# Performance work log

Measured on AMD Instinct MI355X. Metric: run time of the kernel, lower is better.

## Reference

```python
import jax, jax.numpy as jnp
import numpy as np

N_NODES = 100000
N_EDGES = 1600000
F_IN = 256
F_OUT = 128


def setup_inputs() -> dict:
    key = jax.random.key(0)
    k1, k2, k3, k4, k5 = jax.random.split(key, 5)
    x = jax.random.normal(k1, (N_NODES, F_IN), dtype=jnp.float32)
    edge_src = jax.random.randint(k2, (N_EDGES,), 0, N_NODES, dtype=jnp.int64)
    edge_dst = jax.random.randint(k3, (N_EDGES,), 0, N_NODES, dtype=jnp.int64)
    edge_vals = jax.random.uniform(k4, (N_EDGES,), dtype=jnp.float32)
    kernel = jax.random.normal(k5, (F_IN, F_OUT), dtype=jnp.float32) * (1.0 / np.sqrt(F_IN))
    bias = jnp.zeros((F_OUT,), dtype=jnp.float32)
    return {"x": x, "edge_src": edge_src, "edge_dst": edge_dst,
            "edge_vals": edge_vals, "kernel": kernel, "bias": bias}


def reference(x, edge_src, edge_dst, edge_vals, kernel, bias):
    # h = x @ kernel  (dense feature transform), [N, F_OUT]
    h = x @ kernel
    # output = adj @ h  (sparse aggregation over COO edges)
    # message for edge e: adj[dst, src] * h[src]
    msg = h[edge_src] * edge_vals[:, None]          # [E, F_OUT]
    out = jax.ops.segment_sum(msg, edge_dst, num_segments=N_NODES)
    return out + bias
```

## Files before the change

### kernel.cpp

```cpp
#include <hip/hip_runtime.h>

constexpr int F_IN  = 256;
constexpr int F_OUT = 128;

constexpr int BSHIFT = 6;
constexpr int SUPSH  = 5;
constexpr int NPSH   = BSHIFT + SUPSH;
constexpr int NPS    = 1 << NPSH;
constexpr int EPT    = 16;
constexpr int BATCH  = 256 * EPT;
constexpr int CAPS   = 40960;

typedef __attribute__((ext_vector_type(8))) short short8;
typedef __attribute__((ext_vector_type(4))) float f32x4;

__device__ __forceinline__ unsigned short f2bf(float f) {
    unsigned u = __float_as_uint(f);
    u += 0x7fffu + ((u >> 16) & 1u);
    return (unsigned short)(u >> 16);
}

__global__ void prep_wt_kernel(const float* __restrict__ W,
                               unsigned short* __restrict__ Wt,
                               int* __restrict__ cursorA)
{
    int n = blockIdx.x;
    int k = threadIdx.x;
    int ks = k >> 5, kk = k & 31;
    Wt[((ks * F_OUT) + n) * 32 + kk] = f2bf(W[k * F_OUT + n]);
    if (blockIdx.x == 0 && threadIdx.x < 64) cursorA[threadIdx.x] = threadIdx.x * CAPS;
}

#define BS_LD 40

__global__ __launch_bounds__(256) void gemm_mfma_kernel(
    const float* __restrict__ x, const unsigned short* __restrict__ Wt,
    unsigned short* __restrict__ h, int n_nodes)
{
    __shared__ unsigned short Bs[F_OUT * BS_LD];

    const int tid  = threadIdx.x;
    const int wave = tid >> 6;
    const int lane = tid & 63;
    const int m16  = lane & 15;
    const int quad = lane >> 4;
    const int k0q  = quad * 8;
    const int arow = blockIdx.x * 64 + wave * 16 + m16;
    const bool inb = arow < n_nodes;

    f32x4 acc[8];
    #pragma unroll
    for (int t = 0; t < 8; ++t) acc[t] = (f32x4)(0.f);

    float4 a0 = make_float4(0.f,0.f,0.f,0.f), a1 = a0;
    if (inb) {
        a0 = *(const float4*)&x[(long long)arow * F_IN + k0q];
        a1 = *(const float4*)&x[(long long)arow * F_IN + k0q + 4];
    }

    for (int ks = 0; ks < 8; ++ks) {
        const uint4* wsrc = (const uint4*)(Wt + (size_t)ks * F_OUT * 32);
        #pragma unroll
        for (int p = 0; p < 2; ++p) {
            int c   = p * 256 + tid;
            int row = c >> 2;
            int o16 = c & 3;
            *(uint4*)&Bs[row * BS_LD + o16 * 8] = wsrc[c];
        }
        __syncthreads();

        short8 af;
        af[0] = (short)f2bf(a0.x); af[1] = (short)f2bf(a0.y);
        af[2] = (short)f2bf(a0.z); af[3] = (short)f2bf(a0.w);
        af[4] = (short)f2bf(a1.x); af[5] = (short)f2bf(a1.y);
        af[6] = (short)f2bf(a1.z); af[7] = (short)f2bf(a1.w);
        if (!inb) af = (short8)0;

        if (ks < 7 && inb) {
            int kn = (ks + 1) * 32 + k0q;
            a0 = *(const float4*)&x[(long long)arow * F_IN + kn];
            a1 = *(const float4*)&x[(long long)arow * F_IN + kn + 4];
        }

        #pragma unroll
        for (int t = 0; t < 8; ++t) {
            int n = t * 16 + m16;
            short8 bf = *(const short8*)&Bs[n * BS_LD + k0q];
            acc[t] = __builtin_amdgcn_mfma_f32_16x16x32_bf16(af, bf, acc[t], 0, 0, 0);
        }
        __syncthreads();
    }

    const int rbase = blockIdx.x * 64 + wave * 16 + quad * 4;
    #pragma unroll
    for (int r = 0; r < 4; ++r) {
        int grow = rbase + r;
        if (grow < n_nodes) {
            #pragma unroll
            for (int t = 0; t < 8; ++t)
                h[(long long)grow * F_OUT + t * 16 + m16] = f2bf(acc[t][r]);
        }
    }
}

__global__ __launch_bounds__(256) void partition_a_kernel(
    const int* __restrict__ src, const int* __restrict__ dst,
    const float* __restrict__ vals, int* __restrict__ cursorA,
    uint2* __restrict__ payA, int n_edges)
{
    __shared__ int hist[64];
    __shared__ int base[64];
    const int tid = threadIdx.x;
    const int i0  = blockIdx.x * BATCH;

    if (tid < 64) hist[tid] = 0;
    __syncthreads();

    uint2 p[EPT];
    int   sb[EPT];
    int   rk[EPT];
    #pragma unroll
    for (int j = 0; j < EPT; ++j) {
        int i = i0 + j * 256 + tid;
        sb[j] = -1;
        if (i < n_edges) {
            int d = dst[i];
            p[j] = make_uint2((unsigned)src[i] | ((unsigned)(d & (NPS - 1)) << 17),
                              __float_as_uint(vals[i]));
            sb[j] = d >> NPSH;
            rk[j] = atomicAdd(&hist[sb[j]], 1);
        }
    }
    __syncthreads();
    if (tid < 64) { int v = hist[tid]; if (v) base[tid] = atomicAdd(&cursorA[tid], v); }
    __syncthreads();
    #pragma unroll
    for (int j = 0; j < EPT; ++j)
        if (sb[j] >= 0) payA[base[sb[j]] + rk[j]] = p[j];
}

__global__ __launch_bounds__(512) void sort_super_kernel(
    const uint2* __restrict__ payA, const int* __restrict__ super_end,
    uint2* __restrict__ sorted, int* __restrict__ offsets, int n_nodes)
{
    __shared__ int bins[NPS];
    __shared__ int bcur[NPS];
    __shared__ int ss[512];

    const int sp  = blockIdx.x;
    const int tid = threadIdx.x;
    const int lo  = sp * CAPS;
    const int hi  = super_end[sp];

    for (int i = tid; i < NPS; i += 512) bins[i] = 0;
    __syncthreads();

    {
        int e = lo + tid;
        for (; e + 3 * 512 < hi; e += 4 * 512) {
            unsigned x0 = payA[e].x, x1 = payA[e + 512].x,
                     x2 = payA[e + 1024].x, x3 = payA[e + 1536].x;
            atomicAdd(&bins[(x0 >> 17) & (NPS - 1)], 1);
            atomicAdd(&bins[(x1 >> 17) & (NPS - 1)], 1);
            atomicAdd(&bins[(x2 >> 17) & (NPS - 1)], 1);
            atomicAdd(&bins[(x3 >> 17) & (NPS - 1)], 1);
        }
        for (; e < hi; e += 512)
            atomicAdd(&bins[(payA[e].x >> 17) & (NPS - 1)], 1);
    }
    __syncthreads();

    const int b4 = tid * 4;
    int c0 = bins[b4], c1 = bins[b4 + 1], c2 = bins[b4 + 2], c3 = bins[b4 + 3];
    int tot = c0 + c1 + c2 + c3;
    ss[tid] = tot;
    __syncthreads();
    for (int off = 1; off < 512; off <<= 1) {
        int v = (tid >= off) ? ss[tid - off] : 0;
        __syncthreads();
        ss[tid] += v;
        __syncthreads();
    }
    int run = lo + ss[tid] - tot;
    bcur[b4]     = run;
    bcur[b4 + 1] = run + c0;
    bcur[b4 + 2] = run + c0 + c1;
    bcur[b4 + 3] = run + c0 + c1 + c2;
    __syncthreads();

    const int node0 = sp << NPSH;
    for (int i = tid; i < NPS; i += 512) {
        int nd = node0 + i;
        if (nd < n_nodes) offsets[nd] = bcur[i];
    }
    __syncthreads();

    {
        int e = lo + tid;
        for (; e + 3 * 512 < hi; e += 4 * 512) {
            uint2 p0 = payA[e], p1 = payA[e + 512], p2 = payA[e + 1024], p3 = payA[e + 1536];
            int q0 = atomicAdd(&bcur[(p0.x >> 17) & (NPS - 1)], 1);
            int q1 = atomicAdd(&bcur[(p1.x >> 17) & (NPS - 1)], 1);
            int q2 = atomicAdd(&bcur[(p2.x >> 17) & (NPS - 1)], 1);
            int q3 = atomicAdd(&bcur[(p3.x >> 17) & (NPS - 1)], 1);
            sorted[q0] = make_uint2(p0.x & 0x1FFFFu, p0.y);
            sorted[q1] = make_uint2(p1.x & 0x1FFFFu, p1.y);
            sorted[q2] = make_uint2(p2.x & 0x1FFFFu, p2.y);
            sorted[q3] = make_uint2(p3.x & 0x1FFFFu, p3.y);
        }
        for (; e < hi; e += 512) {
            uint2 p = payA[e];
            int q = atomicAdd(&bcur[(p.x >> 17) & (NPS - 1)], 1);
            sorted[q] = make_uint2(p.x & 0x1FFFFu, p.y);
        }
    }
}

__global__ __launch_bounds__(256) void gather_kernel(
    const unsigned short* __restrict__ h, const int* __restrict__ offsets,
    const uint2* __restrict__ sv, const int* __restrict__ super_end,
    const float* __restrict__ bias, float* __restrict__ out, int n_nodes)
{
    int node = blockIdx.x * 4 + (threadIdx.x >> 6);
    if (node >= n_nodes) return;
    int lane = threadIdx.x & 63;
    int f = lane * 2;

    int start = offsets[node];
    int nxt   = node + 1;
    int end   = (nxt == n_nodes || (nxt & (NPS - 1)) == 0)
              ? super_end[node >> NPSH] : offsets[nxt];

    float ax = 0.f, ay = 0.f;

    for (int e = start; e < end; e += 16) {
        uint2 p[16];
        #pragma unroll
        for (int j = 0; j < 16; ++j) {
            int ei = (e + j < end) ? e + j : end - 1;
            p[j] = sv[ei];
        }
        unsigned u[16];
        #pragma unroll
        for (int j = 0; j < 16; ++j)
            u[j] = *(const unsigned*)&h[(size_t)(p[j].x & 0x00FFFFFFu) * F_OUT + f];
        #pragma unroll
        for (int j = 0; j < 16; ++j) {
            float v = (e + j < end) ? __uint_as_float(p[j].y) : 0.f;
            ax += v * __uint_as_float(u[j] << 16);
            ay += v * __uint_as_float(u[j] & 0xffff0000u);
        }
    }

    float2 b = *(const float2*)&bias[f];
    *(float2*)&out[(size_t)node * F_OUT + f] = make_float2(ax + b.x, ay + b.y);
}

extern "C" void kernel_launch(void* const* d_in, const int* in_sizes, int n_in,
                              void* d_out, int out_size, void* d_ws, size_t ws_size,
                              hipStream_t stream)
{
    const float* x     = (const float*)d_in[0];
    const int*   esrc  = (const int*)d_in[1];
    const int*   edst  = (const int*)d_in[2];
    const float* evals = (const float*)d_in[3];
    const float* W     = (const float*)d_in[4];
    const float* bias  = (const float*)d_in[5];
    float*       out   = (float*)d_out;

    const int n_nodes = in_sizes[0] / F_IN;
    const int n_edges = in_sizes[1];
    const int nsup    = (n_nodes + NPS - 1) >> NPSH;

    auto align16 = [](size_t v) { return (v + 15) & ~(size_t)15; };
    char*  base = (char*)d_ws;
    size_t off  = 0;
    unsigned short* h  = (unsigned short*)(base + off); off = align16(off + (size_t)n_nodes * F_OUT * 2);
    unsigned short* Wt = (unsigned short*)(base + off); off = align16(off + (size_t)F_IN * F_OUT * 2);
    int*   cursorA     = (int*)(base + off);   off = align16(off + (size_t)64 * 4);
    int*   offsets     = (int*)(base + off);   off = align16(off + (size_t)n_nodes * 4);
    uint2* payA        = (uint2*)(base + off); off = align16(off + (size_t)nsup * CAPS * 8);
    uint2* sorted      = (uint2*)(base + off); off = align16(off + (size_t)nsup * CAPS * 8);
    (void)ws_size;

    prep_wt_kernel<<<F_OUT, F_IN, 0, stream>>>(W, Wt, cursorA);
    gemm_mfma_kernel<<<(n_nodes + 63) / 64, 256, 0, stream>>>(x, Wt, h, n_nodes);

    partition_a_kernel<<<(n_edges + BATCH - 1) / BATCH, 256, 0, stream>>>(
        esrc, edst, evals, cursorA, payA, n_edges);
    sort_super_kernel<<<nsup, 512, 0, stream>>>(
        payA, cursorA, sorted, offsets, n_nodes);

    gather_kernel<<<(n_nodes + 3) / 4, 256, 0, stream>>>(
        h, offsets, sorted, cursorA, bias, out, n_nodes);
}
```

Baseline: 355.0 us.

## Shrink edge-sort super-buckets to 512 nodes and use nontemporal gather I/O

Cuts each super-bucket from 2048 nodes to 512, which gives 196 buckets instead of 49. The partition kernel now histograms into 256 bins, and the sort kernel gives each of its 512 threads one bin instead of four. The aim is to spread the sort work across many more blocks and keep per-bucket data cache-resident. The gather kernel also reads the sorted edge payload and writes the output with nontemporal hints, so this streamed data does not pollute the cache. The cost is more global atomics on the partition cursors. The fixed per-bucket capacity of 9216 edges leaves less headroom for skewed degree distributions.

```diff
diff --git a/kernel.cpp b/kernel.cpp
--- a/kernel.cpp
+++ b/kernel.cpp
@@ -3,13 +3,11 @@
 constexpr int F_IN  = 256;
 constexpr int F_OUT = 128;
 
-constexpr int BSHIFT = 6;
-constexpr int SUPSH  = 5;
-constexpr int NPSH   = BSHIFT + SUPSH;
-constexpr int NPS    = 1 << NPSH;
-constexpr int EPT    = 16;
-constexpr int BATCH  = 256 * EPT;
-constexpr int CAPS   = 40960;
+constexpr int NPSH  = 9;
+constexpr int NPS   = 1 << NPSH;
+constexpr int EPT   = 16;
+constexpr int BATCH = 256 * EPT;
+constexpr int CAPS  = 9216;
 
 typedef __attribute__((ext_vector_type(8))) short short8;
 typedef __attribute__((ext_vector_type(4))) float f32x4;
@@ -28,7 +26,7 @@
     int k = threadIdx.x;
     int ks = k >> 5, kk = k & 31;
     Wt[((ks * F_OUT) + n) * 32 + kk] = f2bf(W[k * F_OUT + n]);
-    if (blockIdx.x == 0 && threadIdx.x < 64) cursorA[threadIdx.x] = threadIdx.x * CAPS;
+    if (blockIdx.x == 0) cursorA[threadIdx.x] = threadIdx.x * CAPS;
 }
 
 #define BS_LD 40
@@ -108,12 +106,12 @@
     const float* __restrict__ vals, int* __restrict__ cursorA,
     uint2* __restrict__ payA, int n_edges)
 {
-    __shared__ int hist[64];
-    __shared__ int base[64];
+    __shared__ int hist[256];
+    __shared__ int base[256];
     const int tid = threadIdx.x;
     const int i0  = blockIdx.x * BATCH;
 
-    if (tid < 64) hist[tid] = 0;
+    hist[tid] = 0;
     __syncthreads();
 
     uint2 p[EPT];
@@ -132,7 +130,7 @@
         }
     }
     __syncthreads();
-    if (tid < 64) { int v = hist[tid]; if (v) base[tid] = atomicAdd(&cursorA[tid], v); }
+    { int v = hist[tid]; if (v) base[tid] = atomicAdd(&cursorA[tid], v); }
     __syncthreads();
     #pragma unroll
     for (int j = 0; j < EPT; ++j)
@@ -145,14 +143,14 @@
 {
     __shared__ int bins[NPS];
     __shared__ int bcur[NPS];
-    __shared__ int ss[512];
+    __shared__ int ss[NPS];
 
     const int sp  = blockIdx.x;
     const int tid = threadIdx.x;
     const int lo  = sp * CAPS;
     const int hi  = super_end[sp];
 
-    for (int i = tid; i < NPS; i += 512) bins[i] = 0;
+    bins[tid] = 0;
     __syncthreads();
 
     {
@@ -170,10 +168,8 @@
     }
     __syncthreads();
 
-    const int b4 = tid * 4;
-    int c0 = bins[b4], c1 = bins[b4 + 1], c2 = bins[b4 + 2], c3 = bins[b4 + 3];
-    int tot = c0 + c1 + c2 + c3;
-    ss[tid] = tot;
+    const int c0 = bins[tid];
+    ss[tid] = c0;
     __syncthreads();
     for (int off = 1; off < 512; off <<= 1) {
         int v = (tid >= off) ? ss[tid - off] : 0;
@@ -181,17 +177,13 @@
         ss[tid] += v;
         __syncthreads();
     }
-    int run = lo + ss[tid] - tot;
-    bcur[b4]     = run;
-    bcur[b4 + 1] = run + c0;
-    bcur[b4 + 2] = run + c0 + c1;
-    bcur[b4 + 3] = run + c0 + c1 + c2;
+    bcur[tid] = lo + ss[tid] - c0;
     __syncthreads();
 
     const int node0 = sp << NPSH;
-    for (int i = tid; i < NPS; i += 512) {
-        int nd = node0 + i;
-        if (nd < n_nodes) offsets[nd] = bcur[i];
+    {
+        int nd = node0 + tid;
+        if (nd < n_nodes) offsets[nd] = bcur[tid];
     }
     __syncthreads();
 
@@ -234,26 +226,29 @@
     float ax = 0.f, ay = 0.f;
 
     for (int e = start; e < end; e += 16) {
-        uint2 p[16];
+        unsigned long long pv[16];
         #pragma unroll
         for (int j = 0; j < 16; ++j) {
             int ei = (e + j < end) ? e + j : end - 1;
-            p[j] = sv[ei];
+            pv[j] = __builtin_nontemporal_load((const unsigned long long*)&sv[ei]);
         }
         unsigned u[16];
         #pragma unroll
         for (int j = 0; j < 16; ++j)
-            u[j] = *(const unsigned*)&h[(size_t)(p[j].x & 0x00FFFFFFu) * F_OUT + f];
+            u[j] = *(const unsigned*)&h[(size_t)((unsigned)pv[j] & 0x00FFFFFFu) * F_OUT + f];
         #pragma unroll
         for (int j = 0; j < 16; ++j) {
-            float v = (e + j < end) ? __uint_as_float(p[j].y) : 0.f;
+            float v = (e + j < end) ? __uint_as_float((unsigned)(pv[j] >> 32)) : 0.f;
             ax += v * __uint_as_float(u[j] << 16);
             ay += v * __uint_as_float(u[j] & 0xffff0000u);
         }
     }
 
     float2 b = *(const float2*)&bias[f];
-    *(float2*)&out[(size_t)node * F_OUT + f] = make_float2(ax + b.x, ay + b.y);
+    unsigned long long ov =
+        ((unsigned long long)__float_as_uint(ay + b.y) << 32) |
+        (unsigned long long)__float_as_uint(ax + b.x);
+    __builtin_nontemporal_store(ov, (unsigned long long*)&out[(size_t)node * F_OUT + f]);
 }
 
 extern "C" void kernel_launch(void* const* d_in, const int* in_sizes, int n_in,
@@ -277,7 +272,7 @@
     size_t off  = 0;
     unsigned short* h  = (unsigned short*)(base + off); off = align16(off + (size_t)n_nodes * F_OUT * 2);
     unsigned short* Wt = (unsigned short*)(base + off); off = align16(off + (size_t)F_IN * F_OUT * 2);
-    int*   cursorA     = (int*)(base + off);   off = align16(off + (size_t)64 * 4);
+    int*   cursorA     = (int*)(base + off);   off = align16(off + (size_t)256 * 4);
     int*   offsets     = (int*)(base + off);   off = align16(off + (size_t)n_nodes * 4);
     uint2* payA        = (uint2*)(base + off); off = align16(off + (size_t)nsup * CAPS * 8);
     uint2* sorted      = (uint2*)(base + off); off = align16(off + (size_t)nsup * CAPS * 8);
```

Result: faster. 340.6 us (-4.1%).
